# Performance work log

Hardware: AMD Instinct MI355X
Metric: run time of the kernel (lower is better)

## Reference

```python
import jax, jax.numpy as jnp
import numpy as np

B, S, D_MODEL, H, D_K, D_V = 2, 2048, 1024, 16, 64, 64


def setup_inputs() -> dict:
    key = jax.random.key(0)
    ks = jax.random.split(key, 12)
    s = 0.02
    inp = {
        "Q": jax.random.normal(ks[0], (B, S, D_MODEL), jnp.float32),
        "K": jax.random.normal(ks[1], (B, S, D_MODEL), jnp.float32),
        "V": jax.random.normal(ks[2], (B, S, D_MODEL), jnp.float32),
        # causal 0/1 mask, broadcastable to [B, H, S, S]
        "mask": jnp.tril(jnp.ones((S, S), jnp.int32))[None, None, :, :],
        "Wq": jax.random.normal(ks[3], (D_MODEL, H * D_K), jnp.float32) * s,
        "bq": jnp.zeros((H * D_K,), jnp.float32),
        "Wk": jax.random.normal(ks[4], (D_MODEL, H * D_K), jnp.float32) * s,
        "bk": jnp.zeros((H * D_K,), jnp.float32),
        "Wv": jax.random.normal(ks[5], (D_MODEL, H * D_V), jnp.float32) * s,
        "bv": jnp.zeros((H * D_V,), jnp.float32),
        "Wo": jax.random.normal(ks[6], (H * D_V, D_MODEL), jnp.float32) * s,
        "bo": jnp.zeros((D_MODEL,), jnp.float32),
    }
    return inp


def reference(Q, K, V, mask, Wq, bq, Wk, bk, Wv, bv, Wo, bo):
    b = Q.shape[0]
    # project and split heads: [B, S, H*dk] -> [B, H, S, dk]
    q = (Q @ Wq + bq).reshape(b, -1, H, D_K).transpose(0, 2, 1, 3)
    k = (K @ Wk + bk).reshape(b, -1, H, D_K).transpose(0, 2, 1, 3)
    v = (V @ Wv + bv).reshape(b, -1, H, D_V).transpose(0, 2, 1, 3)
    scale = 1.0 / np.sqrt(D_K).astype(np.float32)
    scores = jnp.einsum("bhqd,bhkd->bhqk", q, k) * scale
    scores = jnp.where(mask == 0, jnp.float32(-1e9), scores)
    attn = jax.nn.softmax(scores, axis=-1)
    context = jnp.einsum("bhqk,bhkd->bhqd", attn, v)
    context = context.transpose(0, 2, 1, 3).reshape(b, -1, H * D_V)
    output = context @ Wo + bo  # dropout is identity in eval
    return output, attn
```

## Files before the change

### kernel.cpp

```cpp
#include <hip/hip_runtime.h>
#include <math.h>

#define S_LEN 2048
#define DMODEL 1024
#define NHEAD 16
#define HD 64
#define NBATCH 2

using short8  = __attribute__((ext_vector_type(8))) short;
using ushort8 = __attribute__((ext_vector_type(8))) unsigned short;
using floatx4 = __attribute__((ext_vector_type(4))) float;

__device__ __forceinline__ unsigned short f2b(float f) {
    unsigned int u = __float_as_uint(f);
    unsigned int r = (u + 0x7FFFu + ((u >> 16) & 1u)) >> 16;
    return (unsigned short)r;
}
__device__ __forceinline__ float b2f(unsigned short b) {
    return __uint_as_float(((unsigned int)b) << 16);
}

__device__ __forceinline__ void gll16(const void* g, void* l) {
    __builtin_amdgcn_global_load_lds(
        (const __attribute__((address_space(1))) unsigned int*)g,
        (__attribute__((address_space(3))) unsigned int*)l, 16, 0, 0);
}

__global__ __launch_bounds__(256)
void convert_bf16(const float* __restrict__ S0, const float* __restrict__ S1,
                  const float* __restrict__ S2,
                  unsigned short* __restrict__ D0, unsigned short* __restrict__ D1,
                  unsigned short* __restrict__ D2, int n4)
{
    const float* src = (blockIdx.z == 0) ? S0 : (blockIdx.z == 1) ? S1 : S2;
    unsigned short* dst = (blockIdx.z == 0) ? D0 : (blockIdx.z == 1) ? D1 : D2;
    int i = blockIdx.x * 256 + threadIdx.x;
    if (i < n4) {
        float4 v = ((const float4*)src)[i];
        ushort4 o;
        o.x = f2b(v.x); o.y = f2b(v.y); o.z = f2b(v.z); o.w = f2b(v.w);
        ((ushort4*)dst)[i] = o;
    }
}

__global__ __launch_bounds__(256)
void transpose_w(const float* __restrict__ W0, const float* __restrict__ W1,
                 const float* __restrict__ W2, const float* __restrict__ W3,
                 unsigned short* __restrict__ T0, unsigned short* __restrict__ T1,
                 unsigned short* __restrict__ T2, unsigned short* __restrict__ T3)
{
    __shared__ float t[64][65];
    const float* W; unsigned short* T;
    switch (blockIdx.z) {
        case 0: W = W0; T = T0; break;
        case 1: W = W1; T = T1; break;
        case 2: W = W2; T = T2; break;
        default: W = W3; T = T3; break;
    }
    const int tid = threadIdx.x;
    const int c0 = blockIdx.x * 64;
    const int r0 = blockIdx.y * 64;
    #pragma unroll
    for (int i = 0; i < 4; ++i) {
        int c = tid + i * 256;
        int r = c >> 4, off = (c & 15) * 4;
        float4 v = *(const float4*)(W + (size_t)(r0 + r) * DMODEL + c0 + off);
        t[r][off + 0] = v.x; t[r][off + 1] = v.y;
        t[r][off + 2] = v.z; t[r][off + 3] = v.w;
    }
    __syncthreads();
    #pragma unroll
    for (int i = 0; i < 4; ++i) {
        int c = tid + i * 256;
        int n = c >> 4, off = (c & 15) * 4;
        ushort4 o;
        o.x = f2b(t[off + 0][n]); o.y = f2b(t[off + 1][n]);
        o.z = f2b(t[off + 2][n]); o.w = f2b(t[off + 3][n]);
        *(ushort4*)(T + (size_t)(c0 + n) * DMODEL + r0 + off) = o;
    }
}

__global__ __launch_bounds__(256)
void gemm_qkv(const unsigned short* __restrict__ X0, const unsigned short* __restrict__ X1,
              const unsigned short* __restrict__ X2,
              const unsigned short* __restrict__ W0, const unsigned short* __restrict__ W1,
              const unsigned short* __restrict__ W2,
              const float* __restrict__ b0, const float* __restrict__ b1,
              const float* __restrict__ b2,
              unsigned short* __restrict__ o0, unsigned short* __restrict__ o1,
              unsigned short* __restrict__ o2)
{
    __shared__ unsigned short Xs[128 * 64];
    __shared__ unsigned short Ws[128 * 64];

    const unsigned short* X  = (blockIdx.z == 0) ? X0 : (blockIdx.z == 1) ? X1 : X2;
    const unsigned short* Wt = (blockIdx.z == 0) ? W0 : (blockIdx.z == 1) ? W1 : W2;
    const float* bias        = (blockIdx.z == 0) ? b0 : (blockIdx.z == 1) ? b1 : b2;
    unsigned short* outp     = (blockIdx.z == 0) ? o0 : (blockIdx.z == 1) ? o1 : o2;

    const int tid = threadIdx.x;
    const int lane = tid & 63, w = tid >> 6;
    const int l15 = lane & 15, l4 = lane >> 4;
    const int wr = w >> 1, wc = w & 1;
    const int row0 = blockIdx.y * 128;
    const int col0 = blockIdx.x * 128;

    const int srow = lane >> 3;
    const int sblk = (lane & 7) ^ srow;

    floatx4 acc[4][4] = {};

    for (int k0 = 0; k0 < DMODEL; k0 += 64) {
        __syncthreads();
        #pragma unroll
        for (int i = 0; i < 4; ++i)
            gll16(X + (size_t)(row0 + w * 32 + i * 8 + srow) * DMODEL + k0 + sblk * 8,
                  &Xs[(w * 32 + i * 8) * 64]);
        #pragma unroll
        for (int i = 0; i < 4; ++i)
            gll16(Wt + (size_t)(col0 + w * 32 + i * 8 + srow) * DMODEL + k0 + sblk * 8,
                  &Ws[(w * 32 + i * 8) * 64]);
        asm volatile("s_waitcnt vmcnt(0)" ::: "memory");
        __syncthreads();

        #pragma unroll
        for (int ks = 0; ks < 2; ++ks) {
            short8 a[4], b[4];
            #pragma unroll
            for (int m = 0; m < 4; ++m) {
                const int r = wr * 64 + m * 16 + l15;
                a[m] = *(const short8*)&Xs[r * 64 + (((ks * 4 + l4) ^ (r & 7)) << 3)];
            }
            #pragma unroll
            for (int n = 0; n < 4; ++n) {
                const int r = wc * 64 + n * 16 + l15;
                b[n] = *(const short8*)&Ws[r * 64 + (((ks * 4 + l4) ^ (r & 7)) << 3)];
            }
            #pragma unroll
            for (int m = 0; m < 4; ++m)
                #pragma unroll
                for (int n = 0; n < 4; ++n)
                    acc[m][n] = __builtin_amdgcn_mfma_f32_16x16x32_bf16(
                        a[m], b[n], acc[m][n], 0, 0, 0);
        }
    }

    float bl[4];
    #pragma unroll
    for (int n = 0; n < 4; ++n)
        bl[n] = bias[col0 + wc * 64 + n * 16 + l15];

    #pragma unroll
    for (int m = 0; m < 4; ++m)
        #pragma unroll
        for (int n = 0; n < 4; ++n) {
            const int gc = col0 + wc * 64 + n * 16 + l15;
            const int h = gc >> 6, d = gc & 63;
            #pragma unroll
            for (int reg = 0; reg < 4; ++reg) {
                const int gr = row0 + wr * 64 + m * 16 + l4 * 4 + reg;
                const int bb = gr >> 11, s = gr & 2047;
                outp[(((size_t)bb * NHEAD + h) * S_LEN + s) * HD + d] =
                    f2b(acc[m][n][reg] + bl[n]);
            }
        }
}

__global__ __launch_bounds__(256)
void gemm_out(const unsigned short* __restrict__ X, const unsigned short* __restrict__ Wt,
              const float* __restrict__ bias, float* __restrict__ out)
{
    __shared__ unsigned short Xs[128 * 64];
    __shared__ unsigned short Ws[64 * 64];

    const int tid = threadIdx.x;
    const int lane = tid & 63, w = tid >> 6;
    const int l15 = lane & 15, l4 = lane >> 4;
    const int wr = w >> 1, wc = w & 1;
    const int row0 = blockIdx.y * 128;
    const int col0 = blockIdx.x * 64;

    const int srow = lane >> 3;
    const int sblk = (lane & 7) ^ srow;

    floatx4 acc[4][2] = {};

    for (int k0 = 0; k0 < DMODEL; k0 += 64) {
        __syncthreads();
        #pragma unroll
        for (int i = 0; i < 4; ++i)
            gll16(X + (size_t)(row0 + w * 32 + i * 8 + srow) * DMODEL + k0 + sblk * 8,
                  &Xs[(w * 32 + i * 8) * 64]);
        #pragma unroll
        for (int i = 0; i < 2; ++i)
            gll16(Wt + (size_t)(col0 + w * 16 + i * 8 + srow) * DMODEL + k0 + sblk * 8,
                  &Ws[(w * 16 + i * 8) * 64]);
        asm volatile("s_waitcnt vmcnt(0)" ::: "memory");
        __syncthreads();

        #pragma unroll
        for (int ks = 0; ks < 2; ++ks) {
            short8 a[4], b[2];
            #pragma unroll
            for (int m = 0; m < 4; ++m) {
                const int r = wr * 64 + m * 16 + l15;
                a[m] = *(const short8*)&Xs[r * 64 + (((ks * 4 + l4) ^ (r & 7)) << 3)];
            }
            #pragma unroll
            for (int n = 0; n < 2; ++n) {
                const int r = wc * 32 + n * 16 + l15;
                b[n] = *(const short8*)&Ws[r * 64 + (((ks * 4 + l4) ^ (r & 7)) << 3)];
            }
            #pragma unroll
            for (int m = 0; m < 4; ++m)
                #pragma unroll
                for (int n = 0; n < 2; ++n)
                    acc[m][n] = __builtin_amdgcn_mfma_f32_16x16x32_bf16(
                        a[m], b[n], acc[m][n], 0, 0, 0);
        }
    }

    float bl[2];
    #pragma unroll
    for (int n = 0; n < 2; ++n)
        bl[n] = bias[col0 + wc * 32 + n * 16 + l15];

    #pragma unroll
    for (int m = 0; m < 4; ++m)
        #pragma unroll
        for (int n = 0; n < 2; ++n) {
            const int gc = col0 + wc * 32 + n * 16 + l15;
            #pragma unroll
            for (int reg = 0; reg < 4; ++reg) {
                const int gr = row0 + wr * 64 + m * 16 + l4 * 4 + reg;
                out[(size_t)gr * DMODEL + gc] = acc[m][n][reg] + bl[n];
            }
        }
}

__device__ __forceinline__ int vt_off(int d, int jblk) {
    return d * 64 + ((jblk ^ ((d ^ (d >> 3)) & 7)) << 3);
}

__global__ __launch_bounds__(256)
void attn_mfma(const unsigned short* __restrict__ qg, const unsigned short* __restrict__ kg,
               const unsigned short* __restrict__ vg, float* __restrict__ attn,
               unsigned short* __restrict__ ctx)
{
    __shared__ unsigned short Ks[2 * 64 * 64];
    __shared__ unsigned short Vt[64 * 64];
    __shared__ unsigned short Ps[64 * 88];

    const int tid = threadIdx.x;
    const int lane = tid & 63, w = tid >> 6;
    const int l15 = lane & 15, l4 = lane >> 4;

    const int i0 = blockIdx.x;
    const int local = i0 >> 3;
    const int bh = (i0 & 7) * 4 + (local & 3);
    const int qx = local >> 2;
    const int qb = (bh & 1) ? (31 - qx) : qx;
    const int row0 = qb * 64;

    const int srow = lane >> 3;
    const int sblk = (lane & 7) ^ srow;

    const float C2 = 0.18033688011112042f;

    const unsigned short* qh = qg + (size_t)bh * S_LEN * HD;
    const unsigned short* kh = kg + (size_t)bh * S_LEN * HD;
    const unsigned short* vh = vg + (size_t)bh * S_LEN * HD;
    float* attnh = attn + (size_t)bh * S_LEN * S_LEN;

    short8 qa[2];
    #pragma unroll
    for (int ks = 0; ks < 2; ++ks)
        qa[ks] = *(const short8*)(qh + (size_t)(row0 + w * 16 + l15) * HD + ks * 32 + l4 * 8);

    const int nt = qb + 1;
    const int jj0 = tid >> 3, d0v = (tid & 7) * 8;

    #pragma unroll
    for (int i = 0; i < 2; ++i)
        gll16(kh + (size_t)(w * 16 + i * 8 + srow) * HD + sblk * 8,
              &Ks[(w * 16 + i * 8) * 64]);

    float lsum[4] = {};
    for (int jt = 0; jt < nt; ++jt) {
        const int cur = jt & 1;
        __syncthreads();
        if (jt + 1 < nt) {
            #pragma unroll
            for (int i = 0; i < 2; ++i)
                gll16(kh + (size_t)((jt + 1) * 64 + w * 16 + i * 8 + srow) * HD + sblk * 8,
                      &Ks[(cur ^ 1) * 4096 + (w * 16 + i * 8) * 64]);
            asm volatile("s_waitcnt vmcnt(2)" ::: "memory");
        } else {
            asm volatile("s_waitcnt vmcnt(0)" ::: "memory");
        }
        __syncthreads();

        floatx4 sf[4] = {};
        #pragma unroll
        for (int ks = 0; ks < 2; ++ks) {
            short8 kb[4];
            #pragma unroll
            for (int c = 0; c < 4; ++c) {
                const int r = c * 16 + l15;
                kb[c] = *(const short8*)&Ks[cur * 4096 + r * 64
                                            + (((ks * 4 + l4) ^ (r & 7)) << 3)];
            }
            #pragma unroll
            for (int c = 0; c < 4; ++c)
                sf[c] = __builtin_amdgcn_mfma_f32_16x16x32_bf16(qa[ks], kb[c], sf[c], 0, 0, 0);
        }

        const int rbase = row0 + w * 16;
        if (jt * 64 + 63 <= rbase) {
            #pragma unroll
            for (int c = 0; c < 4; ++c)
                #pragma unroll
                for (int reg = 0; reg < 4; ++reg)
                    lsum[reg] += exp2f(sf[c][reg] * C2);
        } else {
            #pragma unroll
            for (int c = 0; c < 4; ++c) {
                const int jcol = jt * 64 + c * 16 + l15;
                #pragma unroll
                for (int reg = 0; reg < 4; ++reg) {
                    const int grow = rbase + l4 * 4 + reg;
                    lsum[reg] += (jcol <= grow) ? exp2f(sf[c][reg] * C2) : 0.f;
                }
            }
        }
    }

    float nl2[4];
    #pragma unroll
    for (int reg = 0; reg < 4; ++reg) {
        float s = lsum[reg];
        #pragma unroll
        for (int off = 1; off < 16; off <<= 1)
            s += __shfl_xor(s, off);
        nl2[reg] = -__log2f(s);
    }

    floatx4 o[4] = {};

    __syncthreads();
    #pragma unroll
    for (int i = 0; i < 2; ++i)
        gll16(kh + (size_t)(w * 16 + i * 8 + srow) * HD + sblk * 8,
              &Ks[(w * 16 + i * 8) * 64]);
    ushort8 vA0 = *(const ushort8*)(vh + (size_t)jj0 * HD + d0v);
    ushort8 vA1 = *(const ushort8*)(vh + (size_t)(jj0 + 32) * HD + d0v);
    ushort8 vB0, vB1;

    auto p2_iter = [&](int jt, int buf, ushort8& vc0, ushort8& vc1,
                       ushort8& vn0, ushort8& vn1) {
        if (jt + 1 < nt) {
            #pragma unroll
            for (int i = 0; i < 2; ++i)
                gll16(kh + (size_t)((jt + 1) * 64 + w * 16 + i * 8 + srow) * HD + sblk * 8,
                      &Ks[(buf ^ 1) * 4096 + (w * 16 + i * 8) * 64]);
            vn0 = *(const ushort8*)(vh + (size_t)((jt + 1) * 64 + jj0) * HD + d0v);
            vn1 = *(const ushort8*)(vh + (size_t)((jt + 1) * 64 + jj0 + 32) * HD + d0v);
            asm volatile("s_waitcnt vmcnt(4)" ::: "memory");
        } else {
            asm volatile("s_waitcnt vmcnt(0)" ::: "memory");
        }
        __syncthreads();

        #pragma unroll
        for (int e = 0; e < 8; ++e) {
            Vt[vt_off(d0v + e, jj0 >> 3) + (jj0 & 7)] = vc0[e];
            Vt[vt_off(d0v + e, (jj0 + 32) >> 3) + ((jj0 + 32) & 7)] = vc1[e];
        }

        floatx4 sf[4] = {};
        #pragma unroll
        for (int ks = 0; ks < 2; ++ks) {
            short8 kb[4];
            #pragma unroll
            for (int c = 0; c < 4; ++c) {
                const int r = c * 16 + l15;
                kb[c] = *(const short8*)&Ks[buf * 4096 + r * 64
                                            + (((ks * 4 + l4) ^ (r & 7)) << 3)];
            }
            #pragma unroll
            for (int c = 0; c < 4; ++c)
                sf[c] = __builtin_amdgcn_mfma_f32_16x16x32_bf16(qa[ks], kb[c], sf[c], 0, 0, 0);
        }

        const int rbase = row0 + w * 16;
        const bool full = (jt * 64 + 63 <= rbase);
        #pragma unroll
        for (int c = 0; c < 4; ++c) {
            const int jcol = jt * 64 + c * 16 + l15;
            #pragma unroll
            for (int reg = 0; reg < 4; ++reg) {
                const int rl = w * 16 + l4 * 4 + reg;
                float p = exp2f(fmaf(sf[c][reg], C2, nl2[reg]));
                if (!full && jcol > rbase + l4 * 4 + reg) p = 0.f;
                Ps[rl * 88 + c * 16 + l15] = f2b(p);
            }
        }
        __syncthreads();

        #pragma unroll
        for (int i2 = 0; i2 < 4; ++i2) {
            const int idx = tid + i2 * 256;
            const int r = idx >> 4, c4 = (idx & 15) * 4;
            const ushort4 pb = *(const ushort4*)&Ps[r * 88 + c4];
            floatx4 pf;
            pf[0] = b2f(pb.x); pf[1] = b2f(pb.y); pf[2] = b2f(pb.z); pf[3] = b2f(pb.w);
            __builtin_nontemporal_store(
                pf, (floatx4*)(attnh + (size_t)(row0 + r) * S_LEN + jt * 64 + c4));
        }

        #pragma unroll
        for (int ks = 0; ks < 2; ++ks) {
            const short8 pa = *(const short8*)&Ps[(w * 16 + l15) * 88 + ks * 32 + l4 * 8];
            #pragma unroll
            for (int c = 0; c < 4; ++c) {
                const short8 vb = *(const short8*)&Vt[vt_off(c * 16 + l15, ks * 4 + l4)];
                o[c] = __builtin_amdgcn_mfma_f32_16x16x32_bf16(pa, vb, o[c], 0, 0, 0);
            }
        }
    };

    for (int jt2 = 0; jt2 < nt; jt2 += 2) {
        p2_iter(jt2, 0, vA0, vA1, vB0, vB1);
        if (jt2 + 1 < nt)
            p2_iter(jt2 + 1, 1, vB0, vB1, vA0, vA1);
    }

    const int b = bh >> 4, h = bh & 15;
    #pragma unroll
    for (int c = 0; c < 4; ++c)
        #pragma unroll
        for (int reg = 0; reg < 4; ++reg) {
            const int gr = row0 + w * 16 + l4 * 4 + reg;
            const int d = c * 16 + l15;
            ctx[((size_t)b * S_LEN + gr) * DMODEL + h * HD + d] = f2b(o[c][reg]);
        }

    const floatx4 z4 = {0.f, 0.f, 0.f, 0.f};
    for (int jt = nt; jt < S_LEN / 64; ++jt) {
        #pragma unroll
        for (int i = 0; i < 4; ++i) {
            const int idx = tid + i * 256;
            const int r = idx >> 4, off = (idx & 15) * 4;
            __builtin_nontemporal_store(
                z4, (floatx4*)(attnh + (size_t)(row0 + r) * S_LEN + jt * 64 + off));
        }
    }
}

extern "C" void kernel_launch(void* const* d_in, const int* in_sizes, int n_in,
                              void* d_out, int out_size, void* d_ws, size_t ws_size,
                              hipStream_t stream)
{
    const float* Q  = (const float*)d_in[0];
    const float* K  = (const float*)d_in[1];
    const float* V  = (const float*)d_in[2];
    const float* Wq = (const float*)d_in[4];
    const float* bq = (const float*)d_in[5];
    const float* Wk = (const float*)d_in[6];
    const float* bk = (const float*)d_in[7];
    const float* Wv = (const float*)d_in[8];
    const float* bv = (const float*)d_in[9];
    const float* Wo = (const float*)d_in[10];
    const float* bo = (const float*)d_in[11];

    float* out  = (float*)d_out;
    float* attn = out + (size_t)NBATCH * S_LEN * DMODEL;

    const size_t per = (size_t)NBATCH * S_LEN * DMODEL;
    const size_t wsz = (size_t)DMODEL * DMODEL;
    unsigned short* Xq  = (unsigned short*)d_ws;
    unsigned short* Xk  = Xq + per;
    unsigned short* Xv  = Xk + per;
    unsigned short* Wtq = Xv + per;
    unsigned short* Wtk = Wtq + wsz;
    unsigned short* Wtv = Wtk + wsz;
    unsigned short* Wto = Wtv + wsz;
    unsigned short* qhw = Wto + wsz;
    unsigned short* khw = qhw + per;
    unsigned short* vhw = khw + per;
    unsigned short* ctx = vhw + per;

    const int n4 = (int)(per / 4);
    convert_bf16<<<dim3((n4 + 255) / 256, 1, 3), 256, 0, stream>>>(
        Q, K, V, Xq, Xk, Xv, n4);
    transpose_w<<<dim3(16, 16, 4), 256, 0, stream>>>(Wq, Wk, Wv, Wo, Wtq, Wtk, Wtv, Wto);

    gemm_qkv<<<dim3(DMODEL / 128, (NBATCH * S_LEN) / 128, 3), 256, 0, stream>>>(
        Xq, Xk, Xv, Wtq, Wtk, Wtv, bq, bk, bv, qhw, khw, vhw);

    attn_mfma<<<1024, 256, 0, stream>>>(qhw, khw, vhw, attn, ctx);

    gemm_out<<<dim3(DMODEL / 64, (NBATCH * S_LEN) / 128), 256, 0, stream>>>(
        ctx, Wto, bo, out);
}
```

Baseline: 250.3 us.

## Write V projection pre-transposed and load V tiles via direct global-to-LDS copies

The QKV projection epilogue for the V slice (blockIdx.z==2) now stores V in a [bh][d][s] transposed layout with packed 4-element stores. The attention kernel then loads V^T tiles straight into LDS with global_load_lds, the same way as K, and drops the per-element scalar LDS transpose writes and the register double-buffering of V. This removes scattered 2-byte LDS stores and extra VGPR pressure from the inner loop. In exchange the V load is no longer prefetched one tile ahead; it is issued at the start of each iteration and waited on before the PV MFMA.

```diff
diff --git a/kernel.cpp b/kernel.cpp
--- a/kernel.cpp
+++ b/kernel.cpp
@@ -150,20 +150,38 @@
     for (int n = 0; n < 4; ++n)
         bl[n] = bias[col0 + wc * 64 + n * 16 + l15];
 
-    #pragma unroll
-    for (int m = 0; m < 4; ++m)
-        #pragma unroll
-        for (int n = 0; n < 4; ++n) {
-            const int gc = col0 + wc * 64 + n * 16 + l15;
-            const int h = gc >> 6, d = gc & 63;
-            #pragma unroll
-            for (int reg = 0; reg < 4; ++reg) {
-                const int gr = row0 + wr * 64 + m * 16 + l4 * 4 + reg;
-                const int bb = gr >> 11, s = gr & 2047;
-                outp[(((size_t)bb * NHEAD + h) * S_LEN + s) * HD + d] =
-                    f2b(acc[m][n][reg] + bl[n]);
-            }
-        }
+    if (blockIdx.z != 2) {
+        #pragma unroll
+        for (int m = 0; m < 4; ++m)
+            #pragma unroll
+            for (int n = 0; n < 4; ++n) {
+                const int gc = col0 + wc * 64 + n * 16 + l15;
+                const int h = gc >> 6, d = gc & 63;
+                #pragma unroll
+                for (int reg = 0; reg < 4; ++reg) {
+                    const int gr = row0 + wr * 64 + m * 16 + l4 * 4 + reg;
+                    const int bb = gr >> 11, s = gr & 2047;
+                    outp[(((size_t)bb * NHEAD + h) * S_LEN + s) * HD + d] =
+                        f2b(acc[m][n][reg] + bl[n]);
+                }
+            }
+    } else {
+        #pragma unroll
+        for (int m = 0; m < 4; ++m)
+            #pragma unroll
+            for (int n = 0; n < 4; ++n) {
+                const int gc = col0 + wc * 64 + n * 16 + l15;
+                const int h = gc >> 6, d = gc & 63;
+                const int s0 = row0 + wr * 64 + m * 16 + l4 * 4;
+                const int bb = s0 >> 11, sr = s0 & 2047;
+                ushort4 pk;
+                pk.x = f2b(acc[m][n][0] + bl[n]);
+                pk.y = f2b(acc[m][n][1] + bl[n]);
+                pk.z = f2b(acc[m][n][2] + bl[n]);
+                pk.w = f2b(acc[m][n][3] + bl[n]);
+                *(ushort4*)(outp + (((size_t)bb * NHEAD + h) * HD + d) * S_LEN + sr) = pk;
+            }
+    }
 }
 
 __global__ __launch_bounds__(256)
@@ -238,13 +256,9 @@
         }
 }
 
-__device__ __forceinline__ int vt_off(int d, int jblk) {
-    return d * 64 + ((jblk ^ ((d ^ (d >> 3)) & 7)) << 3);
-}
-
 __global__ __launch_bounds__(256)
 void attn_mfma(const unsigned short* __restrict__ qg, const unsigned short* __restrict__ kg,
-               const unsigned short* __restrict__ vg, float* __restrict__ attn,
+               const unsigned short* __restrict__ vtg, float* __restrict__ attn,
                unsigned short* __restrict__ ctx)
 {
     __shared__ unsigned short Ks[2 * 64 * 64];
@@ -269,7 +283,7 @@
 
     const unsigned short* qh = qg + (size_t)bh * S_LEN * HD;
     const unsigned short* kh = kg + (size_t)bh * S_LEN * HD;
-    const unsigned short* vh = vg + (size_t)bh * S_LEN * HD;
+    const unsigned short* vth = vtg + (size_t)bh * HD * S_LEN;
     float* attnh = attn + (size_t)bh * S_LEN * S_LEN;
 
     short8 qa[2];
@@ -278,7 +292,6 @@
         qa[ks] = *(const short8*)(qh + (size_t)(row0 + w * 16 + l15) * HD + ks * 32 + l4 * 8);
 
     const int nt = qb + 1;
-    const int jj0 = tid >> 3, d0v = (tid & 7) * 8;
 
     #pragma unroll
     for (int i = 0; i < 2; ++i)
@@ -352,29 +365,21 @@
     for (int i = 0; i < 2; ++i)
         gll16(kh + (size_t)(w * 16 + i * 8 + srow) * HD + sblk * 8,
               &Ks[(w * 16 + i * 8) * 64]);
-    ushort8 vA0 = *(const ushort8*)(vh + (size_t)jj0 * HD + d0v);
-    ushort8 vA1 = *(const ushort8*)(vh + (size_t)(jj0 + 32) * HD + d0v);
-    ushort8 vB0, vB1;
-
-    auto p2_iter = [&](int jt, int buf, ushort8& vc0, ushort8& vc1,
-                       ushort8& vn0, ushort8& vn1) {
+
+    for (int jt = 0; jt < nt; ++jt) {
+        const int buf = jt & 1;
+        asm volatile("s_waitcnt vmcnt(0)" ::: "memory");
+        __syncthreads();
+
+        #pragma unroll
+        for (int i = 0; i < 2; ++i)
+            gll16(vth + (size_t)(w * 16 + i * 8 + srow) * S_LEN + jt * 64 + sblk * 8,
+                  &Vt[(w * 16 + i * 8) * 64]);
         if (jt + 1 < nt) {
             #pragma unroll
             for (int i = 0; i < 2; ++i)
                 gll16(kh + (size_t)((jt + 1) * 64 + w * 16 + i * 8 + srow) * HD + sblk * 8,
                       &Ks[(buf ^ 1) * 4096 + (w * 16 + i * 8) * 64]);
-            vn0 = *(const ushort8*)(vh + (size_t)((jt + 1) * 64 + jj0) * HD + d0v);
-            vn1 = *(const ushort8*)(vh + (size_t)((jt + 1) * 64 + jj0 + 32) * HD + d0v);
-            asm volatile("s_waitcnt vmcnt(4)" ::: "memory");
-        } else {
-            asm volatile("s_waitcnt vmcnt(0)" ::: "memory");
-        }
-        __syncthreads();
-
-        #pragma unroll
-        for (int e = 0; e < 8; ++e) {
-            Vt[vt_off(d0v + e, jj0 >> 3) + (jj0 & 7)] = vc0[e];
-            Vt[vt_off(d0v + e, (jj0 + 32) >> 3) + ((jj0 + 32) & 7)] = vc1[e];
         }
 
         floatx4 sf[4] = {};
@@ -404,6 +409,11 @@
                 if (!full && jcol > rbase + l4 * 4 + reg) p = 0.f;
                 Ps[rl * 88 + c * 16 + l15] = f2b(p);
             }
+        }
+        if (jt + 1 < nt) {
+            asm volatile("s_waitcnt vmcnt(2)" ::: "memory");
+        } else {
+            asm volatile("s_waitcnt vmcnt(0)" ::: "memory");
         }
         __syncthreads();
 
@@ -423,16 +433,12 @@
             const short8 pa = *(const short8*)&Ps[(w * 16 + l15) * 88 + ks * 32 + l4 * 8];
             #pragma unroll
             for (int c = 0; c < 4; ++c) {
-                const short8 vb = *(const short8*)&Vt[vt_off(c * 16 + l15, ks * 4 + l4)];
+                const int r = c * 16 + l15;
+                const short8 vb = *(const short8*)&Vt[r * 64
+                                                     + (((ks * 4 + l4) ^ (r & 7)) << 3)];
                 o[c] = __builtin_amdgcn_mfma_f32_16x16x32_bf16(pa, vb, o[c], 0, 0, 0);
             }
         }
-    };
-
-    for (int jt2 = 0; jt2 < nt; jt2 += 2) {
-        p2_iter(jt2, 0, vA0, vA1, vB0, vB1);
-        if (jt2 + 1 < nt)
-            p2_iter(jt2 + 1, 1, vB0, vB1, vA0, vA1);
     }
 
     const int b = bh >> 4, h = bh & 15;
```

New measurement: 231.3 us. -7.6%, faster.
